# Kernel optimization log

Hardware: AMD Instinct MI355X
Metric: run time of the kernel (lower is better)

Reference implementation:

```python
import jax, jax.numpy as jnp
import numpy as np
import math

EMBED = 1024
HEADS = 16
HEAD_DIM = EMBED // HEADS
B, S = 2, 2048


def setup_inputs() -> dict:
    key = jax.random.key(0)
    ks = jax.random.split(key, 11)
    s = 1.0 / math.sqrt(EMBED)
    return {
        "query": jax.random.normal(ks[0], (B, S, EMBED), jnp.float32),
        "key_": jax.random.normal(ks[1], (B, S, EMBED), jnp.float32),
        "value": jax.random.normal(ks[2], (B, S, EMBED), jnp.float32),
        "Wq": jax.random.normal(ks[3], (EMBED, EMBED), jnp.float32) * s,
        "bq": jax.random.normal(ks[4], (EMBED,), jnp.float32) * s,
        "Wk": jax.random.normal(ks[5], (EMBED, EMBED), jnp.float32) * s,
        "bk": jax.random.normal(ks[6], (EMBED,), jnp.float32) * s,
        "Wv": jax.random.normal(ks[7], (EMBED, EMBED), jnp.float32) * s,
        "bv": jax.random.normal(ks[8], (EMBED,), jnp.float32) * s,
        "Wo": jax.random.normal(ks[9], (EMBED, EMBED), jnp.float32) * s,
        "bo": jax.random.normal(ks[10], (EMBED,), jnp.float32) * s,
    }


def reference(query, key_, value, Wq, bq, Wk, bk, Wv, bv, Wo, bo):
    b, s, e = query.shape
    # projections (torch Linear: x @ W.T + b)
    q = query @ Wq.T + bq
    k = key_ @ Wk.T + bk
    v = value @ Wv.T + bv
    # [B, H, S, hd]
    q = q.reshape(b, s, HEADS, HEAD_DIM).transpose(0, 2, 1, 3)
    k = k.reshape(b, s, HEADS, HEAD_DIM).transpose(0, 2, 1, 3)
    v = v.reshape(b, s, HEADS, HEAD_DIM).transpose(0, 2, 1, 3)
    scores = jnp.einsum("bhqd,bhkd->bhqk", q, k) / math.sqrt(HEAD_DIM)
    attn = jax.nn.softmax(scores, axis=-1)
    out = jnp.einsum("bhqk,bhkd->bhqd", attn, v)
    out = out.transpose(0, 2, 1, 3).reshape(b, s, e)
    return out @ Wo.T + bo
```

## Files before the change

kernel.cpp:

```cpp
#include <hip/hip_runtime.h>
#include <hip/hip_bf16.h>

using bf16_t = __bf16;
using bf16x2 = __attribute__((ext_vector_type(2))) __bf16;
using bf16x4 = __attribute__((ext_vector_type(4))) __bf16;
using bf16x8 = __attribute__((ext_vector_type(8))) __bf16;
using f32x4  = __attribute__((ext_vector_type(4))) float;
using u32 = unsigned int;
using u32x4 = __attribute__((ext_vector_type(4))) u32;
using i32x2 = __attribute__((ext_vector_type(2))) int;

constexpr int S_ = 2048, E_ = 1024, M_ = 4096;
constexpr size_t MAT_A = (size_t)M_ * E_;
constexpr size_t MAT_W = (size_t)E_ * E_;

__device__ __forceinline__ bf16_t tobf(float f) {
  unsigned u = __builtin_bit_cast(unsigned, f);
  unsigned short r = (unsigned short)((u + 0x7fffu + ((u >> 16) & 1u)) >> 16);
  return __builtin_bit_cast(bf16_t, r);
}
__device__ __forceinline__ u32 packbf2(float a, float b) {
  u32 ua = __builtin_bit_cast(u32, a) + 0x8000u;
  u32 ub = __builtin_bit_cast(u32, b) + 0x8000u;
  return (ua >> 16) | (ub & 0xffff0000u);
}
__device__ __forceinline__ u32 cvtpk(float lo, float hi) {
  bf16x2 t;
  t[0] = (bf16_t)lo;
  t[1] = (bf16_t)hi;
  return __builtin_bit_cast(u32, t);
}
__device__ __forceinline__ void swap32(u32& a, u32& b) {
  i32x2 r = __builtin_amdgcn_permlane32_swap((int)a, (int)b, false, false);
  a = (u32)r[0];
  b = (u32)r[1];
}
__device__ __forceinline__ void swap16(u32& a, u32& b) {
  i32x2 r = __builtin_amdgcn_permlane16_swap((int)a, (int)b, false, false);
  a = (u32)r[0];
  b = (u32)r[1];
}
__device__ __forceinline__ void async_lds16(const bf16_t* g, bf16_t* l) {
  __builtin_amdgcn_global_load_lds(
      (const __attribute__((address_space(1))) unsigned int*)g,
      (__attribute__((address_space(3))) unsigned int*)l, 16, 0, 0);
}

__global__ __launch_bounds__(256) void cvt_all(
    const float* __restrict__ s0, const float* __restrict__ s1,
    const float* __restrict__ s2, const float* __restrict__ s3,
    const float* __restrict__ s4, const float* __restrict__ s5,
    const float* __restrict__ s6,
    bf16_t* __restrict__ d0, bf16_t* __restrict__ d1,
    bf16_t* __restrict__ d2, bf16_t* __restrict__ d3,
    bf16_t* __restrict__ d4, bf16_t* __restrict__ d5,
    bf16_t* __restrict__ d6) {
  size_t i8 = ((size_t)blockIdx.x * 256 + threadIdx.x) * 8;
  const float* s;
  bf16_t* d;
  size_t off;
  if (i8 < 3 * MAT_A) {
    int w = (int)(i8 >> 22);
    off = i8 & (MAT_A - 1);
    s = w == 0 ? s0 : w == 1 ? s1 : s2;
    d = w == 0 ? d0 : w == 1 ? d1 : d2;
  } else {
    size_t j = i8 - 3 * MAT_A;
    int w = (int)(j >> 20);
    off = j & (MAT_W - 1);
    s = w == 0 ? s3 : w == 1 ? s4 : w == 2 ? s5 : s6;
    d = w == 0 ? d3 : w == 1 ? d4 : w == 2 ? d5 : d6;
  }
  float4 a = *(const float4*)(s + off);
  float4 b = *(const float4*)(s + off + 4);
  bf16x8 o;
  o[0] = tobf(a.x); o[1] = tobf(a.y); o[2] = tobf(a.z); o[3] = tobf(a.w);
  o[4] = tobf(b.x); o[5] = tobf(b.y); o[6] = tobf(b.z); o[7] = tobf(b.w);
  *(bf16x8*)(d + off) = o;
}

__global__ __launch_bounds__(256) void gemm_qkv(
    const bf16_t* __restrict__ xq, const bf16_t* __restrict__ xk,
    const bf16_t* __restrict__ xv, const bf16_t* __restrict__ wq,
    const bf16_t* __restrict__ wk, const bf16_t* __restrict__ wv,
    const float* __restrict__ bq, const float* __restrict__ bk,
    const float* __restrict__ bv, bf16_t* __restrict__ outb,
    bf16_t* __restrict__ Vt) {
  constexpr int K = 1024, N = 1024, BK = 64;
  constexpr float SC = 0.18033688011f;
  __shared__ __align__(16) bf16_t smem[2][16384];

  const int which = blockIdx.y >> 3;
  const bf16_t* X = which == 0 ? xq : which == 1 ? xk : xv;
  const bf16_t* W = which == 0 ? wq : which == 1 ? wk : wv;
  const float* bias = which == 0 ? bq : which == 1 ? bk : bv;
  const int row0 = blockIdx.x * 128, col0 = (blockIdx.y & 7) * 128;

  const int tid = threadIdx.x, lane = tid & 63, wave = tid >> 6;
  const int l15 = lane & 15, q = lane >> 4;
  const int wm = (wave & 1) * 64, wn = (wave >> 1) * 64;
  const f32x4 fzero = {0.f, 0.f, 0.f, 0.f};

  f32x4 acc[4][4];
#pragma unroll
  for (int i = 0; i < 4; ++i)
#pragma unroll
    for (int j = 0; j < 4; ++j) acc[i][j] = fzero;

  const int srow = lane >> 3;
  const int schunk = ((lane & 7) ^ srow) * 8;
  const bf16_t* gA = X + (size_t)(row0 + wave * 32 + srow) * K + schunk;
  const bf16_t* gB = W + (size_t)(col0 + wave * 32 + srow) * K + schunk;
  const int lofs = wave * 32 * BK;

  int ck[2];
  ck[0] = ((q) ^ (l15 & 7)) * 8;
  ck[1] = ((4 + q) ^ (l15 & 7)) * 8;

#pragma unroll
  for (int p = 0; p < 4; ++p) {
    async_lds16(gA + (size_t)(p * 8) * K, smem[0] + lofs + p * 8 * BK);
    async_lds16(gB + (size_t)(p * 8) * K, smem[0] + 8192 + lofs + p * 8 * BK);
  }

  for (int it = 0; it < 16; ++it) {
    const int cur = it & 1;
    __syncthreads();
    if (it + 1 < 16) {
      const int k1 = (it + 1) * BK;
      bf16_t* dA = smem[cur ^ 1] + lofs;
      bf16_t* dB = smem[cur ^ 1] + 8192 + lofs;
#pragma unroll
      for (int p = 0; p < 4; ++p) {
        async_lds16(gA + k1 + (size_t)(p * 8) * K, dA + p * 8 * BK);
        async_lds16(gB + k1 + (size_t)(p * 8) * K, dB + p * 8 * BK);
      }
    }
    const bf16_t* As = smem[cur];
    const bf16_t* Bs = smem[cur] + 8192;
#pragma unroll
    for (int h = 0; h < 2; ++h) {
      bf16x8 af[4], bw[4];
#pragma unroll
      for (int i = 0; i < 4; ++i)
        af[i] = *(const bf16x8*)(As + (wm + i * 16 + l15) * BK + ck[h]);
#pragma unroll
      for (int j = 0; j < 4; ++j)
        bw[j] = *(const bf16x8*)(Bs + (wn + j * 16 + l15) * BK + ck[h]);
#pragma unroll
      for (int i = 0; i < 4; ++i)
#pragma unroll
        for (int j = 0; j < 4; ++j)
          acc[i][j] = __builtin_amdgcn_mfma_f32_16x16x32_bf16(af[i], bw[j],
                                                              acc[i][j], 0, 0, 0);
    }
  }

  if (which < 2) {
    const float sc = which == 0 ? SC : 1.0f;
    bf16_t* C = outb + (size_t)which * MAT_A;
#pragma unroll
    for (int j = 0; j < 4; ++j) {
      const int col = col0 + wn + j * 16 + l15;
      const float bc = bias[col];
#pragma unroll
      for (int i = 0; i < 4; ++i)
#pragma unroll
        for (int r = 0; r < 4; ++r) {
          const int row = row0 + wm + i * 16 + q * 4 + r;
          C[(size_t)row * N + col] = tobf((acc[i][j][r] + bc) * sc);
        }
    }
  } else {
    __syncthreads();
    bf16_t* Ep = &smem[0][0] + wave * 4608;
#pragma unroll
    for (int j = 0; j < 4; ++j) {
      const float bc = bias[col0 + wn + j * 16 + l15];
      const int nl = j * 16 + l15;
#pragma unroll
      for (int i = 0; i < 4; ++i) {
        uint2 pk;
        pk.x = packbf2(acc[i][j][0] + bc, acc[i][j][1] + bc);
        pk.y = packbf2(acc[i][j][2] + bc, acc[i][j][3] + bc);
        *(uint2*)(Ep + nl * 72 + i * 16 + q * 4) = pk;
      }
    }
    const int head = (col0 + wn) >> 6;
    const int tok0 = row0 + wm;
    const int bb = tok0 >> 11, tokb = tok0 & 2047;
    const int dl = lane >> 3, ml = (lane & 7) * 8;
#pragma unroll
    for (int p = 0; p < 8; ++p) {
      const int d = dl + p * 8;
      bf16x8 v = *(const bf16x8*)(Ep + d * 72 + ml);
      *(bf16x8*)(Vt + ((size_t)((bb * 16 + head) * 64 + d)) * S_ + tokb + ml) = v;
    }
  }
}

__global__ __launch_bounds__(256) void gemm_o(const bf16_t* __restrict__ X,
                                              const bf16_t* __restrict__ W,
                                              const float* __restrict__ bias,
                                              float* __restrict__ C) {
  constexpr int K = 1024, N = 1024, BK = 64;
  __shared__ __align__(16) bf16_t smem[2][12288];
  const int tid = threadIdx.x, lane = tid & 63, wave = tid >> 6;
  const int l15 = lane & 15, q = lane >> 4;
  const int row0 = blockIdx.x * 64, col0 = blockIdx.y * 128;
  const int wm = (wave & 1) * 32, wn = (wave >> 1) * 64;
  const f32x4 fzero = {0.f, 0.f, 0.f, 0.f};

  f32x4 acc[2][4];
#pragma unroll
  for (int i = 0; i < 2; ++i)
#pragma unroll
    for (int j = 0; j < 4; ++j) acc[i][j] = fzero;

  const int srow = lane >> 3;
  const int schunk = ((lane & 7) ^ srow) * 8;
  const bf16_t* gA = X + (size_t)(row0 + wave * 16 + srow) * K + schunk;
  const bf16_t* gB = W + (size_t)(col0 + wave * 32 + srow) * K + schunk;
  const int lofsA = wave * 16 * BK;
  const int lofsB = wave * 32 * BK;

  int ck[2];
  ck[0] = ((q) ^ (l15 & 7)) * 8;
  ck[1] = ((4 + q) ^ (l15 & 7)) * 8;

  async_lds16(gA, smem[0] + lofsA);
  async_lds16(gA + (size_t)8 * K, smem[0] + lofsA + 8 * BK);
#pragma unroll
  for (int p = 0; p < 4; ++p)
    async_lds16(gB + (size_t)(p * 8) * K, smem[0] + 4096 + lofsB + p * 8 * BK);

  for (int it = 0; it < 16; ++it) {
    const int cur = it & 1;
    __syncthreads();
    if (it + 1 < 16) {
      const int k1 = (it + 1) * BK;
      bf16_t* dA = smem[cur ^ 1] + lofsA;
      bf16_t* dB = smem[cur ^ 1] + 4096 + lofsB;
      async_lds16(gA + k1, dA);
      async_lds16(gA + k1 + (size_t)8 * K, dA + 8 * BK);
#pragma unroll
      for (int p = 0; p < 4; ++p)
        async_lds16(gB + k1 + (size_t)(p * 8) * K, dB + p * 8 * BK);
    }
    const bf16_t* As = smem[cur];
    const bf16_t* Bs = smem[cur] + 4096;
#pragma unroll
    for (int h = 0; h < 2; ++h) {
      bf16x8 af[2], bw[4];
#pragma unroll
      for (int i = 0; i < 2; ++i)
        af[i] = *(const bf16x8*)(As + (wm + i * 16 + l15) * BK + ck[h]);
#pragma unroll
      for (int j = 0; j < 4; ++j)
        bw[j] = *(const bf16x8*)(Bs + (wn + j * 16 + l15) * BK + ck[h]);
#pragma unroll
      for (int i = 0; i < 2; ++i)
#pragma unroll
        for (int j = 0; j < 4; ++j)
          acc[i][j] = __builtin_amdgcn_mfma_f32_16x16x32_bf16(af[i], bw[j],
                                                              acc[i][j], 0, 0, 0);
    }
  }

#pragma unroll
  for (int j = 0; j < 4; ++j) {
    const int col = col0 + wn + j * 16 + l15;
    const float bc = bias[col];
#pragma unroll
    for (int i = 0; i < 2; ++i)
#pragma unroll
      for (int r = 0; r < 4; ++r) {
        const int row = row0 + wm + i * 16 + q * 4 + r;
        C[(size_t)row * N + col] = acc[i][j][r] + bc;
      }
  }
}

__global__ __launch_bounds__(256, 2) void attn_mfma(
    const bf16_t* __restrict__ Qm, const bf16_t* __restrict__ Km,
    const bf16_t* __restrict__ Vtg, bf16_t* __restrict__ Om) {
  __shared__ __align__(16) bf16_t Ks[2][64 * 64];
  __shared__ __align__(16) bf16_t Vs[2][64 * 64];

  const int tid = threadIdx.x, lane = tid & 63, wave = tid >> 6;
  const int l15 = lane & 15, q = lane >> 4;
  const int bh = blockIdx.x & 31, qb = blockIdx.x >> 5;
  const int b = bh >> 4, h = bh & 15;
  const size_t rowbase = (size_t)b * S_;
  const int hcol = h * 64;
  const int q0 = qb * 128 + wave * 32;

  const int srow = lane >> 3;
  const int schunk = (lane & 7) ^ srow;
  const bf16_t* gK = Km + (rowbase + wave * 16 + srow) * E_ + hcol + schunk * 8;
  const bf16_t* gV = Vtg + ((size_t)bh * 64 + wave * 16 + srow) * S_ + schunk * 8;

  bf16x8 qf[2][2];
#pragma unroll
  for (int qt = 0; qt < 2; ++qt) {
    const bf16_t* qp = Qm + (rowbase + q0 + qt * 16 + l15) * E_ + hcol + q * 8;
    qf[qt][0] = *(const bf16x8*)qp;
    qf[qt][1] = *(const bf16x8*)(qp + 32);
  }

  bf16x8 onesv;
#pragma unroll
  for (int j = 0; j < 8; ++j)
    onesv[j] = __builtin_bit_cast(bf16_t, (unsigned short)0x3F80);

  const f32x4 fzero = {0.f, 0.f, 0.f, 0.f};
  f32x4 oacc[2][4];
#pragma unroll
  for (int qt = 0; qt < 2; ++qt)
#pragma unroll
    for (int mt = 0; mt < 4; ++mt) oacc[qt][mt] = fzero;
  f32x4 lsacc[2] = {fzero, fzero};

  const int rbase = l15 * 64;
  int ck[2];
  ck[0] = ((q) ^ (l15 & 7)) * 8;
  ck[1] = ((4 + q) ^ (l15 & 7)) * 8;

  async_lds16(gK, Ks[0] + wave * 1024);
  async_lds16(gK + (size_t)8 * E_, Ks[0] + wave * 1024 + 512);
  async_lds16(gV, Vs[0] + wave * 1024);
  async_lds16(gV + (size_t)8 * S_, Vs[0] + wave * 1024 + 512);

  for (int t = 0; t < 32; ++t) {
    const int pb = t & 1;
    __syncthreads();
    if (t + 1 < 32) {
      const size_t koff = (size_t)((t + 1) * 64) * E_;
      const int voff = (t + 1) * 64;
      bf16_t* dK = Ks[pb ^ 1] + wave * 1024;
      bf16_t* dV = Vs[pb ^ 1] + wave * 1024;
      async_lds16(gK + koff, dK);
      async_lds16(gK + koff + (size_t)8 * E_, dK + 512);
      async_lds16(gV + voff, dV);
      async_lds16(gV + voff + (size_t)8 * S_, dV + 512);
    }
    const bf16_t* Kbuf = Ks[pb];
    const bf16_t* Vbuf = Vs[pb];

    u32 uu[2][4][2];
#pragma unroll
    for (int nt = 0; nt < 4; ++nt) {
      bf16x8 a0 = *(const bf16x8*)(Kbuf + nt * 1024 + rbase + ck[0]);
      bf16x8 a1 = *(const bf16x8*)(Kbuf + nt * 1024 + rbase + ck[1]);
#pragma unroll
      for (int qt = 0; qt < 2; ++qt) {
        f32x4 st = fzero;
        st = __builtin_amdgcn_mfma_f32_16x16x32_bf16(a0, qf[qt][0], st, 0, 0, 0);
        st = __builtin_amdgcn_mfma_f32_16x16x32_bf16(a1, qf[qt][1], st, 0, 0, 0);
        uu[qt][nt][0] =
            cvtpk(__builtin_amdgcn_exp2f(st[0]), __builtin_amdgcn_exp2f(st[1]));
        uu[qt][nt][1] =
            cvtpk(__builtin_amdgcn_exp2f(st[2]), __builtin_amdgcn_exp2f(st[3]));
      }
    }

#pragma unroll
    for (int kk = 0; kk < 2; ++kk) {
      bf16x8 bp[2];
#pragma unroll
      for (int qt = 0; qt < 2; ++qt) {
        u32 A = uu[qt][2 * kk][0], Bv = uu[qt][2 * kk][1];
        u32 C = uu[qt][2 * kk + 1][0], D = uu[qt][2 * kk + 1][1];
        swap32(A, C);  swap16(A, C);
        swap32(Bv, D); swap16(Bv, D);
        u32x4 w = {A, Bv, C, D};
        bp[qt] = __builtin_bit_cast(bf16x8, w);
        lsacc[qt] =
            __builtin_amdgcn_mfma_f32_16x16x32_bf16(onesv, bp[qt], lsacc[qt], 0, 0, 0);
      }
      __builtin_amdgcn_s_setprio(1);
#pragma unroll
      for (int mt = 0; mt < 4; ++mt) {
        bf16x8 av = *(const bf16x8*)(Vbuf + mt * 1024 + rbase + ck[kk]);
        oacc[0][mt] =
            __builtin_amdgcn_mfma_f32_16x16x32_bf16(av, bp[0], oacc[0][mt], 0, 0, 0);
        oacc[1][mt] =
            __builtin_amdgcn_mfma_f32_16x16x32_bf16(av, bp[1], oacc[1][mt], 0, 0, 0);
      }
      __builtin_amdgcn_s_setprio(0);
    }
  }

#pragma unroll
  for (int qt = 0; qt < 2; ++qt) {
    const float inv = 1.0f / lsacc[qt][0];
    const size_t orow = (rowbase + q0 + qt * 16 + l15) * E_ + hcol + q * 4;
#pragma unroll
    for (int mt = 0; mt < 4; ++mt) {
      bf16x4 o;
#pragma unroll
      for (int r = 0; r < 4; ++r) o[r] = tobf(oacc[qt][mt][r] * inv);
      *(bf16x4*)(Om + orow + mt * 16) = o;
    }
  }
}

extern "C" void kernel_launch(void* const* d_in, const int* in_sizes, int n_in,
                              void* d_out, int out_size, void* d_ws, size_t ws_size,
                              hipStream_t stream) {
  const float* query = (const float*)d_in[0];
  const float* key_  = (const float*)d_in[1];
  const float* value = (const float*)d_in[2];
  const float* Wq = (const float*)d_in[3];
  const float* bq = (const float*)d_in[4];
  const float* Wk = (const float*)d_in[5];
  const float* bk = (const float*)d_in[6];
  const float* Wv = (const float*)d_in[7];
  const float* bv = (const float*)d_in[8];
  const float* Wo = (const float*)d_in[9];
  const float* bo = (const float*)d_in[10];

  bf16_t* qc  = (bf16_t*)d_ws;
  bf16_t* kc  = qc + MAT_A;
  bf16_t* vc  = kc + MAT_A;
  bf16_t* wqb = vc + MAT_A;
  bf16_t* wkb = wqb + MAT_W;
  bf16_t* wvb = wkb + MAT_W;
  bf16_t* wob = wvb + MAT_W;
  bf16_t* Qb  = wob + MAT_W;
  bf16_t* Kb  = Qb + MAT_A;
  bf16_t* Vt  = Kb + MAT_A;
  bf16_t* AOb = Vt + MAT_A;

  cvt_all<<<8192, 256, 0, stream>>>(query, key_, value, Wq, Wk, Wv, Wo,
                                    qc, kc, vc, wqb, wkb, wvb, wob);
  gemm_qkv<<<dim3(32, 24), 256, 0, stream>>>(qc, kc, vc, wqb, wkb, wvb,
                                             bq, bk, bv, Qb, Vt);
  attn_mfma<<<512, 256, 0, stream>>>(Qb, Kb, Vt, AOb);
  gemm_o<<<dim3(64, 8), 256, 0, stream>>>(AOb, wob, bo, (float*)d_out);
}
```

Measured before the change: 208.4 us.

## Triple-buffer K/V tiles in attention with prefetch distance two

The attention kernel's K/V shared-memory staging goes from double to triple buffering. Tile t+2 is issued while tile t is computed, and the full barrier is replaced by an explicit partial vmcnt wait plus s_barrier, so the load for the next tile can stay in flight across the barrier. The aim is to hide more global-memory latency behind the MFMA work. In exchange, LDS per block grows from 32KB to 48KB, and correctness now relies on the hand-counted vmcnt values.

```diff
diff --git a/kernel.cpp b/kernel.cpp
--- a/kernel.cpp
+++ b/kernel.cpp
@@ -284,8 +284,8 @@
 __global__ __launch_bounds__(256, 2) void attn_mfma(
     const bf16_t* __restrict__ Qm, const bf16_t* __restrict__ Km,
     const bf16_t* __restrict__ Vtg, bf16_t* __restrict__ Om) {
-  __shared__ __align__(16) bf16_t Ks[2][64 * 64];
-  __shared__ __align__(16) bf16_t Vs[2][64 * 64];
+  __shared__ __align__(16) bf16_t Ks[3][64 * 64];
+  __shared__ __align__(16) bf16_t Vs[3][64 * 64];
 
   const int tid = threadIdx.x, lane = tid & 63, wave = tid >> 6;
   const int l15 = lane & 15, q = lane >> 4;
@@ -326,27 +326,18 @@
   ck[0] = ((q) ^ (l15 & 7)) * 8;
   ck[1] = ((4 + q) ^ (l15 & 7)) * 8;
 
-  async_lds16(gK, Ks[0] + wave * 1024);
-  async_lds16(gK + (size_t)8 * E_, Ks[0] + wave * 1024 + 512);
-  async_lds16(gV, Vs[0] + wave * 1024);
-  async_lds16(gV + (size_t)8 * S_, Vs[0] + wave * 1024 + 512);
-
-  for (int t = 0; t < 32; ++t) {
-    const int pb = t & 1;
-    __syncthreads();
-    if (t + 1 < 32) {
-      const size_t koff = (size_t)((t + 1) * 64) * E_;
-      const int voff = (t + 1) * 64;
-      bf16_t* dK = Ks[pb ^ 1] + wave * 1024;
-      bf16_t* dV = Vs[pb ^ 1] + wave * 1024;
-      async_lds16(gK + koff, dK);
-      async_lds16(gK + koff + (size_t)8 * E_, dK + 512);
-      async_lds16(gV + voff, dV);
-      async_lds16(gV + voff + (size_t)8 * S_, dV + 512);
-    }
-    const bf16_t* Kbuf = Ks[pb];
-    const bf16_t* Vbuf = Vs[pb];
-
+  auto STAGE = [&](int tile, int bi) {
+    const size_t koff = (size_t)(tile * 64) * E_;
+    const int voff = tile * 64;
+    bf16_t* dK = Ks[bi] + wave * 1024;
+    bf16_t* dV = Vs[bi] + wave * 1024;
+    async_lds16(gK + koff, dK);
+    async_lds16(gK + koff + (size_t)8 * E_, dK + 512);
+    async_lds16(gV + voff, dV);
+    async_lds16(gV + voff + (size_t)8 * S_, dV + 512);
+  };
+
+  auto COMPUTE = [&](const bf16_t* Kbuf, const bf16_t* Vbuf) {
     u32 uu[2][4][2];
 #pragma unroll
     for (int nt = 0; nt < 4; ++nt) {
@@ -363,7 +354,6 @@
             cvtpk(__builtin_amdgcn_exp2f(st[2]), __builtin_amdgcn_exp2f(st[3]));
       }
     }
-
 #pragma unroll
     for (int kk = 0; kk < 2; ++kk) {
       bf16x8 bp[2];
@@ -375,21 +365,42 @@
         swap32(Bv, D); swap16(Bv, D);
         u32x4 w = {A, Bv, C, D};
         bp[qt] = __builtin_bit_cast(bf16x8, w);
-        lsacc[qt] =
-            __builtin_amdgcn_mfma_f32_16x16x32_bf16(onesv, bp[qt], lsacc[qt], 0, 0, 0);
+        lsacc[qt] = __builtin_amdgcn_mfma_f32_16x16x32_bf16(onesv, bp[qt],
+                                                            lsacc[qt], 0, 0, 0);
       }
       __builtin_amdgcn_s_setprio(1);
 #pragma unroll
       for (int mt = 0; mt < 4; ++mt) {
         bf16x8 av = *(const bf16x8*)(Vbuf + mt * 1024 + rbase + ck[kk]);
-        oacc[0][mt] =
-            __builtin_amdgcn_mfma_f32_16x16x32_bf16(av, bp[0], oacc[0][mt], 0, 0, 0);
-        oacc[1][mt] =
-            __builtin_amdgcn_mfma_f32_16x16x32_bf16(av, bp[1], oacc[1][mt], 0, 0, 0);
+        oacc[0][mt] = __builtin_amdgcn_mfma_f32_16x16x32_bf16(av, bp[0],
+                                                              oacc[0][mt], 0, 0, 0);
+        oacc[1][mt] = __builtin_amdgcn_mfma_f32_16x16x32_bf16(av, bp[1],
+                                                              oacc[1][mt], 0, 0, 0);
       }
       __builtin_amdgcn_s_setprio(0);
     }
-  }
+  };
+
+  STAGE(0, 0);
+  STAGE(1, 1);
+
+  int cur = 0;
+  for (int t = 0; t < 31; ++t) {
+    asm volatile("s_waitcnt vmcnt(4)" ::: "memory");
+    __builtin_amdgcn_sched_barrier(0);
+    __builtin_amdgcn_s_barrier();
+    if (t + 2 < 32) {
+      int nb = cur + 2;
+      if (nb >= 3) nb -= 3;
+      STAGE(t + 2, nb);
+    }
+    COMPUTE(Ks[cur], Vs[cur]);
+    cur = cur == 2 ? 0 : cur + 1;
+  }
+  asm volatile("s_waitcnt vmcnt(0)" ::: "memory");
+  __builtin_amdgcn_sched_barrier(0);
+  __builtin_amdgcn_s_barrier();
+  COMPUTE(Ks[cur], Vs[cur]);
 
 #pragma unroll
   for (int qt = 0; qt < 2; ++qt) {
```

Result: no change. 208.1 us (-0.2%).
